# Kernel tuning notes

Measured on AMD Instinct MI355X. Metric: run time of the kernel, lower is better.

The kernel has to match this reference:

```python
import jax, jax.numpy as jnp
import numpy as np

N_NODES = 50000
N_EDGES = 1600000
D = 64
L = 4
ALPHA = 0.1


def setup_inputs() -> dict:
    key = jax.random.key(0)
    ks = jax.random.split(key, 6)
    x = jax.random.normal(ks[0], (N_NODES, D), dtype=jnp.float32)
    w = jax.random.uniform(ks[1], (N_EDGES,), dtype=jnp.float32)
    # linear layer params, scaled ~ 1/sqrt(fan_in)
    W = jax.random.normal(ks[2], (L, D, D), dtype=jnp.float32) * (1.0 / np.sqrt(D))
    b = jnp.zeros((L, D), dtype=jnp.float32)
    # GPR temp schedule: alpha*(1-alpha)^k, last = (1-alpha)^L
    temp = ALPHA * (1.0 - ALPHA) ** np.arange(L + 1)
    temp[-1] = (1.0 - ALPHA) ** L
    temp = jnp.asarray(temp, dtype=jnp.float32)
    src = jax.random.randint(ks[3], (N_EDGES,), 0, N_NODES, dtype=jnp.int32)
    dst = jax.random.randint(ks[4], (N_EDGES,), 0, N_NODES, dtype=jnp.int32)
    return {"x": x, "w": w, "W": W, "b": b, "temp": temp, "src": src, "dst": dst}


def reference(x, w, W, b, temp, src, dst):
    # Eval mode: dropout / dropout_adj are identity; edge_attn=False.
    n = x.shape[0]
    hidden = x * temp[0]
    num_layers = W.shape[0]
    for i in range(num_layers):
        # linear: h = x @ W_i^T + b_i
        h = jnp.einsum('nd,od->no', x, W[i]) + b[i]
        # u_mul_e + sum: gather src features, scale by edge weight, scatter-sum to dst
        m = h[src] * w[:, None]                       # [E, D]
        x = jax.ops.segment_sum(m, dst, num_segments=n)  # [N, D]
        x = jax.nn.relu(x)
        hidden = hidden + x * temp[i + 1]
    return hidden
```

## Files before the change

### kernel.cpp

```cpp
#include <hip/hip_runtime.h>
#include <hip/hip_fp16.h>

#define NN 50000
#define NE 1600000
#define DD 64
#define NBK 782
#define TILE 4096
#define NTB 391
#define SCAP 3072

typedef _Float16 half8 __attribute__((ext_vector_type(8)));
typedef float float4v __attribute__((ext_vector_type(4)));

__global__ __launch_bounds__(256) void wswz_kernel(const float* __restrict__ W,
                                                   _Float16* __restrict__ Wswz,
                                                   int* __restrict__ gcur) {
    int flat = blockIdx.x * 256 + threadIdx.x;
    if (blockIdx.x == 0) {
        for (int k = threadIdx.x; k < NBK; k += 256) gcur[k] = 0;
    }
    int l = flat >> 12, r = flat & 4095;
    int j = r & 7, lane = (r >> 3) & 63, kt = (r >> 9) & 1, nt = r >> 10;
    int n = nt * 16 + (lane & 15);
    int k = kt * 32 + ((lane >> 4) * 8) + j;
    Wswz[flat] = (_Float16)W[l * 4096 + n * 64 + k];
}

__global__ __launch_bounds__(256) void fill_kernel(const int* __restrict__ src,
                                                   const int* __restrict__ dst,
                                                   const float* __restrict__ w,
                                                   int* __restrict__ gcur,
                                                   unsigned int* __restrict__ tmp) {
    __shared__ unsigned int data[TILE];
    __shared__ unsigned short bktl[TILE];
    __shared__ int cnt[NBK], bas[NBK], rnk[NBK];
    __shared__ int sc[1024];
    int t = threadIdx.x;
    for (int k = t; k < NBK; k += 256) { cnt[k] = 0; rnk[k] = 0; }
    __syncthreads();
    int base = blockIdx.x * TILE;
    unsigned int er_e[TILE / 256];
    int er_b[TILE / 256];
#pragma unroll
    for (int kk = 0; kk < 4; ++kk) {
        int i0 = base + kk * 1024 + t * 4;
        if (i0 + 3 < NE) {
            int4   d4 = *(const int4*)(dst + i0);
            int4   s4 = *(const int4*)(src + i0);
            float4 w4 = *(const float4*)(w + i0);
            const int*   dp = (const int*)&d4;
            const int*   sp = (const int*)&s4;
            const float* wp = (const float*)&w4;
#pragma unroll
            for (int u = 0; u < 4; ++u) {
                int d = dp[u];
                unsigned int wq = (unsigned int)(wp[u] * 1024.0f);
                if (wq > 1023u) wq = 1023u;
                er_e[kk * 4 + u] = (unsigned int)sp[u] | ((unsigned int)(d & 63) << 16) | (wq << 22);
                er_b[kk * 4 + u] = d >> 6;
                atomicAdd(&cnt[d >> 6], 1);
            }
        } else {
#pragma unroll
            for (int u = 0; u < 4; ++u) {
                int i = i0 + u;
                if (i < NE) {
                    int d = dst[i];
                    unsigned int wq = (unsigned int)(w[i] * 1024.0f);
                    if (wq > 1023u) wq = 1023u;
                    er_e[kk * 4 + u] = (unsigned int)src[i] | ((unsigned int)(d & 63) << 16) | (wq << 22);
                    er_b[kk * 4 + u] = d >> 6;
                    atomicAdd(&cnt[d >> 6], 1);
                } else {
                    er_b[kk * 4 + u] = -1;
                }
            }
        }
    }
    __syncthreads();
    for (int k = t; k < NBK; k += 256) {
        int c = cnt[k];
        bas[k] = c ? atomicAdd(&gcur[k], c) : 0;
    }
    for (int k = t; k < 1024; k += 256) sc[k] = (k < NBK) ? cnt[k] : 0;
    __syncthreads();
    for (int s = 1; s < 1024; s <<= 1) {
        int v0[4];
#pragma unroll
        for (int j = 0; j < 4; ++j) {
            int idx = t + j * 256;
            v0[j] = (idx >= s) ? sc[idx - s] : 0;
        }
        __syncthreads();
#pragma unroll
        for (int j = 0; j < 4; ++j) sc[t + j * 256] += v0[j];
        __syncthreads();
    }
#pragma unroll
    for (int k = 0; k < TILE / 256; ++k) {
        if (er_b[k] >= 0) {
            int b = er_b[k];
            int r = atomicAdd(&rnk[b], 1);
            int pos = (sc[b] - cnt[b]) + r;
            data[pos] = er_e[k];
            bktl[pos] = (unsigned short)b;
        }
    }
    __syncthreads();
    int tot = NE - base; if (tot > TILE) tot = TILE;
    for (int idx = t; idx < tot; idx += 256) {
        int b = bktl[idx];
        int lb = sc[b] - cnt[b];
        tmp[(size_t)b * SCAP + bas[b] + (idx - lb)] = data[idx];
    }
}

__global__ __launch_bounds__(256) void sortgemm_kernel(const unsigned int* __restrict__ tmp,
                                                       const int* __restrict__ gcur,
                                                       unsigned int* __restrict__ csr,
                                                       int2* __restrict__ off2,
                                                       const float* __restrict__ x32,
                                                       const _Float16* __restrict__ Wg,
                                                       const float* __restrict__ bl,
                                                       _Float16* __restrict__ h) {
    __shared__ unsigned int sdata[SCAP];
    __shared__ int cnt[64], nb[64], pos[64];
    int b = blockIdx.x, t = threadIdx.x;

    int wave = t >> 6, lane = t & 63;
    int m = lane & 15, q = lane >> 4;
    int node0 = b * 64 + wave * 16;
    int arow = node0 + m; if (arow >= NN) arow = NN - 1;
    const float4* xr = (const float4*)(x32 + (size_t)arow * 64);
    float4 f0 = xr[2 * q], f1 = xr[2 * q + 1];
    float4 f2 = xr[8 + 2 * q], f3 = xr[8 + 2 * q + 1];

    int beg = b * SCAP, n = gcur[b];
    if (t < 64) cnt[t] = 0;
    __syncthreads();
    for (int i = t; i < n; i += 256) {
        unsigned int e = tmp[beg + i];
        sdata[i] = e;
        atomicAdd(&cnt[(e >> 16) & 63u], 1);
    }
    __syncthreads();
    if (t == 0) {
        int a = 0;
        for (int k = 0; k < 64; ++k) { nb[k] = a; pos[k] = a; a += cnt[k]; }
    }
    __syncthreads();
    for (int i = t; i < n; i += 256) {
        unsigned int e = sdata[i];
        int d = (int)((e >> 16) & 63u);
        float wf = ((float)(e >> 22) + 0.5f) * (1.0f / 1024.0f);
        unsigned int wh = (unsigned int)__half_as_ushort(__float2half_rn(wf));
        int r = atomicAdd(&pos[d], 1);
        csr[beg + r] = (e & 0xffffu) | (wh << 16);
    }
    if (t < 64) {
        int node = b * 64 + t;
        if (node < NN) {
            int2 oe;
            oe.x = beg + nb[t];
            oe.y = beg + nb[t] + cnt[t];
            off2[node] = oe;
        }
    }

    half8 a0, a1;
    a0[0] = (_Float16)f0.x; a0[1] = (_Float16)f0.y; a0[2] = (_Float16)f0.z; a0[3] = (_Float16)f0.w;
    a0[4] = (_Float16)f1.x; a0[5] = (_Float16)f1.y; a0[6] = (_Float16)f1.z; a0[7] = (_Float16)f1.w;
    a1[0] = (_Float16)f2.x; a1[1] = (_Float16)f2.y; a1[2] = (_Float16)f2.z; a1[3] = (_Float16)f2.w;
    a1[4] = (_Float16)f3.x; a1[5] = (_Float16)f3.y; a1[6] = (_Float16)f3.z; a1[7] = (_Float16)f3.w;
    const half8* Wf = (const half8*)Wg;
    float4v acc[4];
#pragma unroll
    for (int nt = 0; nt < 4; ++nt) acc[nt] = (float4v){0.f, 0.f, 0.f, 0.f};
#pragma unroll
    for (int nt = 0; nt < 4; ++nt) {
        half8 b0 = Wf[(nt * 2 + 0) * 64 + lane];
        half8 b1 = Wf[(nt * 2 + 1) * 64 + lane];
        acc[nt] = __builtin_amdgcn_mfma_f32_16x16x32_f16(a0, b0, acc[nt], 0, 0, 0);
        acc[nt] = __builtin_amdgcn_mfma_f32_16x16x32_f16(a1, b1, acc[nt], 0, 0, 0);
    }
#pragma unroll
    for (int nt = 0; nt < 4; ++nt) {
        float bv = bl[nt * 16 + m];
#pragma unroll
        for (int r = 0; r < 4; ++r) {
            int node = node0 + q * 4 + r;
            if (node < NN)
                h[(size_t)node * 64 + nt * 16 + m] = (_Float16)(acc[nt][r] + bv);
        }
    }
}

__global__ __launch_bounds__(256) void pull_fused(const uint4* __restrict__ h16,
                                                  const unsigned int* __restrict__ csr,
                                                  const int2* __restrict__ off2,
                                                  float4* __restrict__ out,
                                                  const float4* __restrict__ x32,
                                                  const float* __restrict__ temp,
                                                  const _Float16* __restrict__ Wg,
                                                  const float* __restrict__ bl,
                                                  _Float16* __restrict__ hout,
                                                  int layer) {
    __shared__ _Float16 vsh[16 * 72];
    int t = threadIdx.x;
    int lane = t & 63;
    int slot = lane >> 4, g = (lane >> 3) & 1, sub = lane & 7;
    int node0 = blockIdx.x * 16;
    int nloc = (t >> 6) * 4 + slot;
    int node = node0 + nloc;
    bool tail = (node0 + 16 > NN);
    if (tail) {
        for (int k = t; k < 16 * 72; k += 256) vsh[k] = (_Float16)0.f;
        __syncthreads();
    }

    int nclamp = node < NN ? node : NN - 1;
    int2 oe = off2[nclamp];
    int deg = (node < NN) ? (oe.y - oe.x) : 0;
    int beg = oe.x;
    int dmax = deg;
    dmax = max(dmax, __shfl_xor(dmax, 16));
    dmax = max(dmax, __shfl_xor(dmax, 32));
    int sl = lane & 15;
    float acc[8];
#pragma unroll
    for (int k = 0; k < 8; ++k) acc[k] = 0.f;

    int chunks = (dmax + 15) >> 4;
    unsigned int e = (sl < deg) ? csr[beg + sl] : 0u;
    for (int c = 0; c < chunks; ++c) {
        int nidx = ((c + 1) << 4) + sl;
        unsigned int enext = (nidx < deg) ? csr[beg + nidx] : 0u;
#pragma unroll
        for (int j = 0; j < 8; ++j) {
            unsigned int ej = (unsigned int)__shfl((int)e, (slot << 4) + j * 2 + g);
            int s = (int)(ej & 0xffffu);
            __half wh = __ushort_as_half((unsigned short)(ej >> 16));
            uint4 hv = h16[(size_t)s * 8 + sub];
            const __half* hp = (const __half*)&hv;
            float wf = (float)wh;
#pragma unroll
            for (int k = 0; k < 8; ++k)
                acc[k] += (float)hp[k] * wf;
        }
        e = enext;
    }
#pragma unroll
    for (int k = 0; k < 8; ++k) acc[k] += __shfl_xor(acc[k], 8);

    if (g == 0 && node < NN) {
        float tk = temp[layer + 1];
        float v[8];
#pragma unroll
        for (int k = 0; k < 8; ++k) v[k] = fmaxf(acc[k], 0.f);
        __half2 p[4];
#pragma unroll
        for (int k = 0; k < 4; ++k) p[k] = __floats2half2_rn(v[2 * k], v[2 * k + 1]);
        *(uint4*)&vsh[nloc * 72 + sub * 8] = *(const uint4*)p;
        int gi = node * 16 + sub * 2;
        float4 o0, o1;
        if (layer == 0) {
            float t0 = temp[0];
            float4 a = x32[gi], bq = x32[gi + 1];
            o0.x = a.x * t0;  o0.y = a.y * t0;  o0.z = a.z * t0;  o0.w = a.w * t0;
            o1.x = bq.x * t0; o1.y = bq.y * t0; o1.z = bq.z * t0; o1.w = bq.w * t0;
        } else {
            o0 = out[gi]; o1 = out[gi + 1];
        }
        o0.x += v[0] * tk; o0.y += v[1] * tk; o0.z += v[2] * tk; o0.w += v[3] * tk;
        o1.x += v[4] * tk; o1.y += v[5] * tk; o1.z += v[6] * tk; o1.w += v[7] * tk;
        out[gi]     = o0;
        out[gi + 1] = o1;
    }

    if (Wg != nullptr) {
        __syncthreads();
        int wave = t >> 6;
        int m = lane & 15, q = lane >> 4;
        half8 a0 = *(const half8*)&vsh[m * 72 + q * 8];
        half8 a1 = *(const half8*)&vsh[m * 72 + 32 + q * 8];
        const half8* Wf = (const half8*)Wg;
        half8 b0 = Wf[(wave * 2 + 0) * 64 + lane];
        half8 b1 = Wf[(wave * 2 + 1) * 64 + lane];
        float4v d = (float4v){0.f, 0.f, 0.f, 0.f};
        d = __builtin_amdgcn_mfma_f32_16x16x32_f16(a0, b0, d, 0, 0, 0);
        d = __builtin_amdgcn_mfma_f32_16x16x32_f16(a1, b1, d, 0, 0, 0);
        float bv = bl[wave * 16 + m];
#pragma unroll
        for (int r = 0; r < 4; ++r) {
            int n2 = node0 + q * 4 + r;
            if (n2 < NN)
                hout[(size_t)n2 * 64 + wave * 16 + m] = (_Float16)(d[r] + bv);
        }
    }
}

extern "C" void kernel_launch(void* const* d_in, const int* in_sizes, int n_in,
                              void* d_out, int out_size, void* d_ws, size_t ws_size,
                              hipStream_t stream) {
    const float* x    = (const float*)d_in[0];
    const float* w    = (const float*)d_in[1];
    const float* W    = (const float*)d_in[2];
    const float* b    = (const float*)d_in[3];
    const float* temp = (const float*)d_in[4];
    const int*   src  = (const int*)d_in[5];
    const int*   dst  = (const int*)d_in[6];
    float* out = (float*)d_out;

    _Float16*     hA   = (_Float16*)d_ws;
    _Float16*     hB   = hA + (size_t)NN * DD;
    unsigned int* csr  = (unsigned int*)(hB + (size_t)NN * DD);
    unsigned int* tmp  = csr + (size_t)NBK * SCAP;
    int*          gcur = (int*)(tmp + (size_t)NBK * SCAP);
    int2*         off2 = (int2*)(gcur + NBK);
    _Float16*     Wswz = (_Float16*)(off2 + NN);

    wswz_kernel<<<64, 256, 0, stream>>>(W, Wswz, gcur);
    fill_kernel<<<NTB, 256, 0, stream>>>(src, dst, w, gcur, tmp);
    sortgemm_kernel<<<NBK, 256, 0, stream>>>(tmp, gcur, csr, off2, x, Wswz, b, hA);

    const int PG = (NN + 15) / 16;
    _Float16* hin  = hA;
    _Float16* hout = hB;
    for (int l = 0; l < 4; ++l) {
        const _Float16* Wn = (l < 3) ? (Wswz + (size_t)(l + 1) * 4096) : nullptr;
        const float*    bn = (l < 3) ? (b + (size_t)(l + 1) * DD) : nullptr;
        pull_fused<<<PG, 256, 0, stream>>>(
            (const uint4*)hin, csr, off2, (float4*)out, (const float4*)x,
            temp, Wn, bn, hout, l);
        _Float16* sw = hin; hin = hout; hout = sw;
    }
}
```

Before: 224.2 us.

## Split feature dimension into two half passes for cache-resident gathers

Stores h in a split layout of two 32-column halves and runs the gather/aggregate kernel twice per layer, once per half, so each pass's gather working set (50000x32 fp16) is smaller and more likely to stay cache-resident. The first half's ReLU output goes through a global vtmp buffer, and the second pass does the fused GEMM using both halves. The running hidden sum is kept in fp16 in a workspace buffer and written to the fp32 output only at the last layer. This doubles the CSR traversal and the launch count, and lowers the precision of the accumulated hidden sum.

```diff
diff --git a/kernel.cpp b/kernel.cpp
--- a/kernel.cpp
+++ b/kernel.cpp
@@ -10,6 +10,7 @@
 #define SCAP 3072
 
 typedef _Float16 half8 __attribute__((ext_vector_type(8)));
+typedef _Float16 half4 __attribute__((ext_vector_type(4)));
 typedef float float4v __attribute__((ext_vector_type(4)));
 
 __global__ __launch_bounds__(256) void wswz_kernel(const float* __restrict__ W,
@@ -190,12 +191,13 @@
         for (int r = 0; r < 4; ++r) {
             int node = node0 + q * 4 + r;
             if (node < NN)
-                h[(size_t)node * 64 + nt * 16 + m] = (_Float16)(acc[nt][r] + bv);
-        }
-    }
-}
-
-__global__ __launch_bounds__(256) void pull_fused(const uint4* __restrict__ h16,
+                h[(size_t)(nt >> 1) * NN * 32 + (size_t)node * 32 + (nt & 1) * 16 + m] =
+                    (_Float16)(acc[nt][r] + bv);
+        }
+    }
+}
+
+__global__ __launch_bounds__(256) void pull_fused(const _Float16* __restrict__ hin,
                                                   const unsigned int* __restrict__ csr,
                                                   const int2* __restrict__ off2,
                                                   float4* __restrict__ out,
@@ -204,7 +206,9 @@
                                                   const _Float16* __restrict__ Wg,
                                                   const float* __restrict__ bl,
                                                   _Float16* __restrict__ hout,
-                                                  int layer) {
+                                                  _Float16* __restrict__ hid,
+                                                  _Float16* __restrict__ vtmp,
+                                                  int half, int layer) {
     __shared__ _Float16 vsh[16 * 72];
     int t = threadIdx.x;
     int lane = t & 63;
@@ -212,11 +216,6 @@
     int node0 = blockIdx.x * 16;
     int nloc = (t >> 6) * 4 + slot;
     int node = node0 + nloc;
-    bool tail = (node0 + 16 > NN);
-    if (tail) {
-        for (int k = t; k < 16 * 72; k += 256) vsh[k] = (_Float16)0.f;
-        __syncthreads();
-    }
 
     int nclamp = node < NN ? node : NN - 1;
     int2 oe = off2[nclamp];
@@ -226,10 +225,11 @@
     dmax = max(dmax, __shfl_xor(dmax, 16));
     dmax = max(dmax, __shfl_xor(dmax, 32));
     int sl = lane & 15;
-    float acc[8];
-#pragma unroll
-    for (int k = 0; k < 8; ++k) acc[k] = 0.f;
-
+    float acc[4];
+#pragma unroll
+    for (int k = 0; k < 4; ++k) acc[k] = 0.f;
+
+    const uint2* hh = (const uint2*)(hin + (size_t)half * NN * 32);
     int chunks = (dmax + 15) >> 4;
     unsigned int e = (sl < deg) ? csr[beg + sl] : 0u;
     for (int c = 0; c < chunks; ++c) {
@@ -240,48 +240,61 @@
             unsigned int ej = (unsigned int)__shfl((int)e, (slot << 4) + j * 2 + g);
             int s = (int)(ej & 0xffffu);
             __half wh = __ushort_as_half((unsigned short)(ej >> 16));
-            uint4 hv = h16[(size_t)s * 8 + sub];
+            uint2 hv = hh[(size_t)s * 8 + sub];
             const __half* hp = (const __half*)&hv;
             float wf = (float)wh;
 #pragma unroll
-            for (int k = 0; k < 8; ++k)
+            for (int k = 0; k < 4; ++k)
                 acc[k] += (float)hp[k] * wf;
         }
         e = enext;
     }
 #pragma unroll
-    for (int k = 0; k < 8; ++k) acc[k] += __shfl_xor(acc[k], 8);
+    for (int k = 0; k < 4; ++k) acc[k] += __shfl_xor(acc[k], 8);
 
     if (g == 0 && node < NN) {
         float tk = temp[layer + 1];
-        float v[8];
-#pragma unroll
-        for (int k = 0; k < 8; ++k) v[k] = fmaxf(acc[k], 0.f);
-        __half2 p[4];
-#pragma unroll
-        for (int k = 0; k < 4; ++k) p[k] = __floats2half2_rn(v[2 * k], v[2 * k + 1]);
-        *(uint4*)&vsh[nloc * 72 + sub * 8] = *(const uint4*)p;
-        int gi = node * 16 + sub * 2;
-        float4 o0, o1;
+        float v[4];
+#pragma unroll
+        for (int k = 0; k < 4; ++k) v[k] = fmaxf(acc[k], 0.f);
+        half4 pv;
+#pragma unroll
+        for (int k = 0; k < 4; ++k) pv[k] = (_Float16)v[k];
+        if (half == 0) {
+            *(half4*)&vtmp[(size_t)node * 32 + sub * 4] = pv;
+        } else {
+            *(half4*)&vsh[nloc * 72 + 32 + sub * 4] = pv;
+        }
+        float hv[4];
         if (layer == 0) {
             float t0 = temp[0];
-            float4 a = x32[gi], bq = x32[gi + 1];
-            o0.x = a.x * t0;  o0.y = a.y * t0;  o0.z = a.z * t0;  o0.w = a.w * t0;
-            o1.x = bq.x * t0; o1.y = bq.y * t0; o1.z = bq.z * t0; o1.w = bq.w * t0;
+            float4 a = x32[node * 16 + half * 8 + sub];
+#pragma unroll
+            for (int k = 0; k < 4; ++k)
+                hv[k] = ((const float*)&a)[k] * t0 + v[k] * tk;
         } else {
-            o0 = out[gi]; o1 = out[gi + 1];
-        }
-        o0.x += v[0] * tk; o0.y += v[1] * tk; o0.z += v[2] * tk; o0.w += v[3] * tk;
-        o1.x += v[4] * tk; o1.y += v[5] * tk; o1.z += v[6] * tk; o1.w += v[7] * tk;
-        out[gi]     = o0;
-        out[gi + 1] = o1;
+            half4 prev = *(const half4*)&hid[(size_t)node * 64 + half * 32 + sub * 4];
+#pragma unroll
+            for (int k = 0; k < 4; ++k) hv[k] = (float)prev[k] + v[k] * tk;
+        }
+        if (layer == 3) {
+            float4 o;
+            o.x = hv[0]; o.y = hv[1]; o.z = hv[2]; o.w = hv[3];
+            out[node * 16 + half * 8 + sub] = o;
+        } else {
+            half4 st;
+#pragma unroll
+            for (int k = 0; k < 4; ++k) st[k] = (_Float16)hv[k];
+            *(half4*)&hid[(size_t)node * 64 + half * 32 + sub * 4] = st;
+        }
     }
 
     if (Wg != nullptr) {
         __syncthreads();
         int wave = t >> 6;
         int m = lane & 15, q = lane >> 4;
-        half8 a0 = *(const half8*)&vsh[m * 72 + q * 8];
+        int arow = node0 + m; if (arow >= NN) arow = NN - 1;
+        half8 a0 = *(const half8*)&vtmp[(size_t)arow * 32 + q * 8];
         half8 a1 = *(const half8*)&vsh[m * 72 + 32 + q * 8];
         const half8* Wf = (const half8*)Wg;
         half8 b0 = Wf[(wave * 2 + 0) * 64 + lane];
@@ -294,7 +307,8 @@
         for (int r = 0; r < 4; ++r) {
             int n2 = node0 + q * 4 + r;
             if (n2 < NN)
-                hout[(size_t)n2 * 64 + wave * 16 + m] = (_Float16)(d[r] + bv);
+                hout[(size_t)(wave >> 1) * NN * 32 + (size_t)n2 * 32 + (wave & 1) * 16 + m] =
+                    (_Float16)(d[r] + bv);
         }
     }
 }
@@ -318,6 +332,8 @@
     int*          gcur = (int*)(tmp + (size_t)NBK * SCAP);
     int2*         off2 = (int2*)(gcur + NBK);
     _Float16*     Wswz = (_Float16*)(off2 + NN);
+    _Float16*     hid  = (_Float16*)tmp;
+    _Float16*     vtmp = hid + (size_t)NN * DD;
 
     wswz_kernel<<<64, 256, 0, stream>>>(W, Wswz, gcur);
     fill_kernel<<<NTB, 256, 0, stream>>>(src, dst, w, gcur, tmp);
@@ -330,8 +346,11 @@
         const _Float16* Wn = (l < 3) ? (Wswz + (size_t)(l + 1) * 4096) : nullptr;
         const float*    bn = (l < 3) ? (b + (size_t)(l + 1) * DD) : nullptr;
         pull_fused<<<PG, 256, 0, stream>>>(
-            (const uint4*)hin, csr, off2, (float4*)out, (const float4*)x,
-            temp, Wn, bn, hout, l);
+            hin, csr, off2, (float4*)out, (const float4*)x,
+            temp, nullptr, nullptr, nullptr, hid, vtmp, 0, l);
+        pull_fused<<<PG, 256, 0, stream>>>(
+            hin, csr, off2, (float4*)out, (const float4*)x,
+            temp, Wn, bn, hout, hid, vtmp, 1, l);
         _Float16* sw = hin; hin = hout; hout = sw;
     }
 }
```

Result: slower. 261.4 us (+16.6%).
